# Performance work log

Measured on AMD Instinct MI355X. Metric: run time of the kernel, lower is better.

## Reference

```python
import jax, jax.numpy as jnp
import numpy as np

D_MODEL = 1024
N_HEADS = 16
D_HEAD = D_MODEL // N_HEADS
B, S = 4, 2048


def setup_inputs() -> dict:
    key = jax.random.key(0)
    ks = jax.random.split(key, 12)
    std = 1.0 / np.sqrt(D_MODEL)
    inp = {
        "q": jax.random.normal(ks[0], (B, S, D_MODEL), jnp.float32),
        "k": jax.random.normal(ks[1], (B, S, D_MODEL), jnp.float32),
        "v": jax.random.normal(ks[2], (B, S, D_MODEL), jnp.float32),
        # causal mask: 1 where attention is disallowed (j > i)
        "mask": jnp.triu(jnp.ones((S, S), jnp.int32), k=1)[None, None],
        "Wq": jax.random.normal(ks[3], (D_MODEL, D_MODEL), jnp.float32) * std,
        "bq": jnp.zeros((D_MODEL,), jnp.float32),
        "Wk": jax.random.normal(ks[4], (D_MODEL, D_MODEL), jnp.float32) * std,
        "bk": jnp.zeros((D_MODEL,), jnp.float32),
        "Wv": jax.random.normal(ks[5], (D_MODEL, D_MODEL), jnp.float32) * std,
        "bv": jnp.zeros((D_MODEL,), jnp.float32),
        "Wo": jax.random.normal(ks[6], (D_MODEL, D_MODEL), jnp.float32) * std,
        "bo": jnp.zeros((D_MODEL,), jnp.float32),
    }
    return inp


def _split_heads(x):
    # [B, S, D] -> [B, H, S, d_head]
    b, s, _ = x.shape
    return x.reshape(b, s, N_HEADS, D_HEAD).transpose(0, 2, 1, 3)


def reference(q, k, v, mask, Wq, bq, Wk, bk, Wv, bv, Wo, bo):
    # torch Linear: y = x @ W.T + b
    qh = _split_heads(q @ Wq.T + bq)
    kh = _split_heads(k @ Wk.T + bk)
    vh = _split_heads(v @ Wv.T + bv)
    # NOTE: original scales by sqrt(d_model), not sqrt(d_head)
    scale = 1.0 / np.sqrt(D_MODEL).astype(np.float32)
    logits = jnp.einsum("bhqd,bhkd->bhqk", qh, kh) * scale
    logits = logits + mask.astype(logits.dtype) * (-1e9)
    weights = jax.nn.softmax(logits, axis=-1)
    attn = jnp.einsum("bhqk,bhkd->bhqd", weights, vh)
    attn = attn.transpose(0, 2, 1, 3).reshape(q.shape[0], -1, D_MODEL)
    out = attn @ Wo.T + bo
    return out, weights
```

## Files before the change

### kernel.cpp

```cpp
#include <hip/hip_runtime.h>
#include <stdint.h>

typedef unsigned short u16;
typedef __attribute__((ext_vector_type(8))) short bf16x8;
typedef __attribute__((ext_vector_type(8))) unsigned short us8;
typedef __attribute__((ext_vector_type(4))) float f32x4;

typedef __attribute__((address_space(1))) void as1_void;
typedef __attribute__((address_space(3))) void as3_void;

#define S_LEN 2048
#define DMODEL 1024
#define DH 64
#define NHEADS 16
#define NB 4
#define GM (NB * S_LEN)
#define GN DMODEL
#define GK DMODEL
#define SCALE 0.03125f

__device__ __forceinline__ void gload16(const void* g, void* l) {
  __builtin_amdgcn_global_load_lds((const as1_void*)g, (as3_void*)l, 16, 0, 0);
}
__device__ __forceinline__ float bf2f(u16 u) {
  union { unsigned int i; float f; } x; x.i = ((unsigned int)u) << 16; return x.f;
}
__device__ __forceinline__ u16 f2bf(float f) {
  union { float f; unsigned int i; } x; x.f = f;
  unsigned int u = x.i + 0x7fffu + ((x.i >> 16) & 1u);
  return (u16)(u >> 16);
}
__device__ __forceinline__ f32x4 mfma16(bf16x8 a, bf16x8 b, f32x4 c) {
  return __builtin_amdgcn_mfma_f32_16x16x32_bf16(a, b, c, 0, 0, 0);
}
__device__ __forceinline__ void nt_store4(f32x4 v, float* p) {
  __builtin_nontemporal_store(v, (f32x4*)p);
}

__device__ __forceinline__ void cvt_chunk(const float* s, u16* d, int i) {
  const f32x4 a = *(const f32x4*)(s + (size_t)i * 8);
  const f32x4 b = *(const f32x4*)(s + (size_t)i * 8 + 4);
  us8 o;
  o[0] = f2bf(a[0]); o[1] = f2bf(a[1]); o[2] = f2bf(a[2]); o[3] = f2bf(a[3]);
  o[4] = f2bf(b[0]); o[5] = f2bf(b[1]); o[6] = f2bf(b[2]); o[7] = f2bf(b[3]);
  *(us8*)(d + (size_t)i * 8) = o;
}
__global__ __launch_bounds__(256)
void cvt3(const float* __restrict__ s0, const float* __restrict__ s1,
          const float* __restrict__ s2, u16* __restrict__ d0,
          u16* __restrict__ d1, u16* __restrict__ d2, int n8) {
  const int i = blockIdx.x * 256 + threadIdx.x;
  if (i >= n8) return;
  const float* s; u16* d;
  if (blockIdx.y == 0)      { s = s0; d = d0; }
  else if (blockIdx.y == 1) { s = s1; d = d1; }
  else                      { s = s2; d = d2; }
  cvt_chunk(s, d, i);
}
__global__ __launch_bounds__(256)
void cvt4(const float* __restrict__ s0, const float* __restrict__ s1,
          const float* __restrict__ s2, const float* __restrict__ s3,
          u16* __restrict__ d0, u16* __restrict__ d1,
          u16* __restrict__ d2, u16* __restrict__ d3, int n8) {
  const int i = blockIdx.x * 256 + threadIdx.x;
  if (i >= n8) return;
  const float* s; u16* d;
  if (blockIdx.y == 0)      { s = s0; d = d0; }
  else if (blockIdx.y == 1) { s = s1; d = d1; }
  else if (blockIdx.y == 2) { s = s2; d = d2; }
  else                      { s = s3; d = d3; }
  cvt_chunk(s, d, i);
}

template<bool OUTF>
__device__ __forceinline__ void gemm_body(const u16* __restrict__ A,
                                          const u16* __restrict__ W,
                                          const float* __restrict__ bias,
                                          void* __restrict__ Cv,
                                          u16* smem) {
  u16* As = smem;
  u16* Bs = smem + 2 * 8192;
  const int tid  = threadIdx.x;
  const int lane = tid & 63;
  const int wv   = tid >> 6;
  const int wr   = wv >> 1, wc = wv & 1;
  const int rlow = lane & 15, rhi = lane >> 4;
  const int m0 = blockIdx.x * 128;
  const int n0 = blockIdx.y * 128;

  f32x4 acc[4][4];
#pragma unroll
  for (int i = 0; i < 4; ++i)
#pragma unroll
    for (int j = 0; j < 4; ++j) acc[i][j] = (f32x4){0.f, 0.f, 0.f, 0.f};

#define STAGE_G(bufi, kk)                                                     \
  {                                                                           \
    _Pragma("unroll")                                                         \
    for (int i = 0; i < 4; ++i) {                                             \
      const int c = i * 256 + tid;                                            \
      const int row = c >> 3, cw = c & 7;                                     \
      const int koff = ((kk) << 6) + ((cw ^ (row & 7)) << 3);                 \
      gload16(A + (size_t)(m0 + row) * GK + koff,                             \
              &As[(bufi) * 8192 + ((c - lane) << 3)]);                        \
      gload16(W + (size_t)(n0 + row) * GK + koff,                             \
              &Bs[(bufi) * 8192 + ((c - lane) << 3)]);                        \
    }                                                                         \
  }

  const int nk = GK >> 6;
  STAGE_G(0, 0);
  __syncthreads();
  int buf = 0;
  for (int kk = 0; kk < nk; ++kk) {
    if (kk + 1 < nk) STAGE_G(buf ^ 1, kk + 1);
    const u16* Ab = &As[buf * 8192];
    const u16* Bb = &Bs[buf * 8192];
    bf16x8 af[4][2], bfr[4][2];
#pragma unroll
    for (int mi = 0; mi < 4; ++mi) {
      const int row = wr * 64 + mi * 16 + rlow;
#pragma unroll
      for (int k2 = 0; k2 < 2; ++k2)
        af[mi][k2] = *(const bf16x8*)&Ab[row * 64 + (((rhi + k2 * 4) ^ (row & 7)) << 3)];
    }
#pragma unroll
    for (int ni = 0; ni < 4; ++ni) {
      const int row = wc * 64 + ni * 16 + rlow;
#pragma unroll
      for (int k2 = 0; k2 < 2; ++k2)
        bfr[ni][k2] = *(const bf16x8*)&Bb[row * 64 + (((rhi + k2 * 4) ^ (row & 7)) << 3)];
    }
#pragma unroll
    for (int mi = 0; mi < 4; ++mi)
#pragma unroll
      for (int ni = 0; ni < 4; ++ni) {
        acc[mi][ni] = mfma16(af[mi][0], bfr[ni][0], acc[mi][ni]);
        acc[mi][ni] = mfma16(af[mi][1], bfr[ni][1], acc[mi][ni]);
      }
    __syncthreads();
    buf ^= 1;
  }
#undef STAGE_G

  if constexpr (OUTF) {
    float* Cs = (float*)smem;
#pragma unroll
    for (int ni = 0; ni < 4; ++ni) {
      const int col = wc * 64 + ni * 16 + rlow;
      const float bv = bias[n0 + col];
#pragma unroll
      for (int mi = 0; mi < 4; ++mi)
#pragma unroll
        for (int r = 0; r < 4; ++r)
          Cs[(wr * 64 + mi * 16 + rhi * 4 + r) * 128 + col] = acc[mi][ni][r] + bv;
    }
    __syncthreads();
#pragma unroll
    for (int i = 0; i < 16; ++i) {
      const int c = i * 256 + tid;
      const int row = c >> 5, cw = c & 31;
      const f32x4 t = *(const f32x4*)&Cs[row * 128 + cw * 4];
      nt_store4(t, &((float*)Cv)[(size_t)(m0 + row) * GN + n0 + cw * 4]);
    }
  } else {
    u16* Cs = smem;
#pragma unroll
    for (int ni = 0; ni < 4; ++ni) {
      const int col = wc * 64 + ni * 16 + rlow;
      const float bv = bias[n0 + col];
#pragma unroll
      for (int mi = 0; mi < 4; ++mi)
#pragma unroll
        for (int r = 0; r < 4; ++r)
          Cs[(wr * 64 + mi * 16 + rhi * 4 + r) * 144 + col] = f2bf(acc[mi][ni][r] + bv);
    }
    __syncthreads();
#pragma unroll
    for (int i = 0; i < 8; ++i) {
      const int c = i * 256 + tid;
      const int row = c >> 4, cw = c & 15;
      const us8 t = *(const us8*)&Cs[row * 144 + cw * 8];
      *(us8*)&((u16*)Cv)[(size_t)(m0 + row) * GN + n0 + cw * 8] = t;
    }
  }
}

__global__ __launch_bounds__(256, 2)
void gemm_qkv(const u16* __restrict__ xq, const u16* __restrict__ xk,
              const u16* __restrict__ xv, const u16* __restrict__ wq,
              const u16* __restrict__ wk, const u16* __restrict__ wv,
              const float* __restrict__ bq, const float* __restrict__ bk,
              const float* __restrict__ bv, u16* __restrict__ oq,
              u16* __restrict__ ok, u16* __restrict__ ov) {
  __shared__ u16 smem[4 * 8192];
  const u16 *A, *W; const float* bias; u16* C;
  if (blockIdx.z == 0)      { A = xq; W = wq; bias = bq; C = oq; }
  else if (blockIdx.z == 1) { A = xk; W = wk; bias = bk; C = ok; }
  else                      { A = xv; W = wv; bias = bv; C = ov; }
  gemm_body<false>(A, W, bias, C, smem);
}

__global__ __launch_bounds__(256, 2)
void gemm_o(const u16* __restrict__ A, const u16* __restrict__ W,
            const float* __restrict__ bias, float* __restrict__ C) {
  __shared__ u16 smem[4 * 8192];
  gemm_body<true>(A, W, bias, C, smem);
}

__global__ __launch_bounds__(512, 4)
void attn_fused(const u16* __restrict__ qh, const u16* __restrict__ kh,
                const u16* __restrict__ vh, float* __restrict__ wout,
                u16* __restrict__ am)
{
  __shared__ u16 smem[34304];
  u16* Ws  = smem;
  u16* Qs  = smem;
  u16* Kb1 = smem;
  u16* Kb0 = smem + 17408;
  u16* VT  = smem + 17408 + 8192;

  const int tid = threadIdx.x, lane = tid & 63, wv = tid >> 6;
  const int rlow = lane & 15, rhi = lane >> 4;
  const int idx = blockIdx.x;
  const int bh  = idx & 63;
  const int qt  = 15 - (idx >> 6);
  const int b = bh >> 4, h = bh & 15;
  const int q0 = qt << 7;
  const size_t headoff = (size_t)b * S_LEN * DMODEL + h * DH;

#define STAGE_K(dst, jtile)                                                   \
  {                                                                           \
    _Pragma("unroll")                                                         \
    for (int i = 0; i < 2; ++i) {                                             \
      const int c = i * 512 + tid;                                            \
      const int row = c >> 3, cw = c & 7;                                     \
      gload16(kh + headoff + (size_t)((jtile) * 128 + row) * DMODEL +         \
              ((cw ^ (row & 7)) << 3), &(dst)[(c - lane) << 3]);              \
    }                                                                         \
  }

#pragma unroll
  for (int i = 0; i < 2; ++i) {
    const int c = i * 512 + tid;
    const int row = c >> 3, cw = c & 7;
    gload16(qh + headoff + (size_t)(q0 + row) * DMODEL + ((cw ^ (row & 7)) << 3),
            &Qs[(c - lane) << 3]);
  }
  __syncthreads();
  bf16x8 qf[2];
  {
    const int row = wv * 16 + rlow;
#pragma unroll
    for (int k2 = 0; k2 < 2; ++k2)
      qf[k2] = *(const bf16x8*)&Qs[row * 64 + (((rhi + k2 * 4) ^ (row & 7)) << 3)];
  }

  const int gi_base = q0 + wv * 16 + rhi * 4;
  float ssum[4] = {0.f, 0.f, 0.f, 0.f};

  STAGE_K(Kb0, 0);
  for (int jt = 0; jt <= qt; ++jt) {
    __syncthreads();
    const u16* kcur = (jt & 1) ? Kb1 : Kb0;
    if (jt < qt) {
      u16* knxt = (jt & 1) ? Kb0 : Kb1;
      STAGE_K(knxt, jt + 1);
    }
    const bool diag = (jt == qt);
    float pexp[4] = {0.f, 0.f, 0.f, 0.f};
#pragma unroll
    for (int half = 0; half < 2; ++half) {
      f32x4 acc[4];
#pragma unroll
      for (int ni = 0; ni < 4; ++ni) acc[ni] = (f32x4){0.f, 0.f, 0.f, 0.f};
#pragma unroll
      for (int k2 = 0; k2 < 2; ++k2) {
#pragma unroll
        for (int ni = 0; ni < 4; ++ni) {
          const int row = (half * 4 + ni) * 16 + rlow;
          bf16x8 kf = *(const bf16x8*)&kcur[row * 64 + (((rhi + k2 * 4) ^ (row & 7)) << 3)];
          acc[ni] = mfma16(qf[k2], kf, acc[ni]);
        }
      }
#pragma unroll
      for (int ni = 0; ni < 4; ++ni) {
        const int gj = jt * 128 + (half * 4 + ni) * 16 + rlow;
#pragma unroll
        for (int r = 0; r < 4; ++r) {
          if (!diag || gj <= gi_base + r) pexp[r] += __expf(acc[ni][r] * SCALE);
        }
      }
    }
#pragma unroll
    for (int r = 0; r < 4; ++r) {
      float p = pexp[r];
      p += __shfl_xor(p, 1);
      p += __shfl_xor(p, 2);
      p += __shfl_xor(p, 4);
      p += __shfl_xor(p, 8);
      ssum[r] += p;
    }
  }
  float inv_s[4];
#pragma unroll
  for (int r = 0; r < 4; ++r) inv_s[r] = 1.f / ssum[r];

  f32x4 opv[4];
#pragma unroll
  for (int ni = 0; ni < 4; ++ni) opv[ni] = (f32x4){0.f, 0.f, 0.f, 0.f};

  for (int jt = 0; jt <= qt; ++jt) {
    __syncthreads();
    STAGE_K(Kb0, jt);
#pragma unroll
    for (int i = 0; i < 2; ++i) {
      const int j = (i << 6) | lane;
      const int d0v = wv << 3;
      bf16x8 vv = *(const bf16x8*)(vh + headoff + (size_t)(jt * 128 + j) * DMODEL + d0v);
#pragma unroll
      for (int e = 0; e < 8; ++e) VT[(d0v + e) * 136 + j] = (u16)vv[e];
    }
    __syncthreads();
    const bool diag = (jt == qt);
#pragma unroll
    for (int half = 0; half < 2; ++half) {
      f32x4 acc[4];
#pragma unroll
      for (int ni = 0; ni < 4; ++ni) acc[ni] = (f32x4){0.f, 0.f, 0.f, 0.f};
#pragma unroll
      for (int k2 = 0; k2 < 2; ++k2) {
#pragma unroll
        for (int ni = 0; ni < 4; ++ni) {
          const int row = (half * 4 + ni) * 16 + rlow;
          bf16x8 kf = *(const bf16x8*)&Kb0[row * 64 + (((rhi + k2 * 4) ^ (row & 7)) << 3)];
          acc[ni] = mfma16(qf[k2], kf, acc[ni]);
        }
      }
#pragma unroll
      for (int ni = 0; ni < 4; ++ni) {
        const int col = (half * 4 + ni) * 16 + rlow;
        const int gj = jt * 128 + col;
#pragma unroll
        for (int r = 0; r < 4; ++r) {
          float w = 0.f;
          if (!diag || gj <= gi_base + r) w = __expf(acc[ni][r] * SCALE) * inv_s[r];
          Ws[(wv * 16 + rhi * 4 + r) * 136 + col] = f2bf(w);
        }
      }
    }
    __syncthreads();
    {
      const size_t wbase = ((size_t)bh * S_LEN + q0) * S_LEN + (size_t)jt * 128;
#pragma unroll
      for (int i = 0; i < 8; ++i) {
        const int c = i * 512 + tid;
        const int row = c >> 5, cw = c & 31;
        f32x4 t;
        t[0] = bf2f(Ws[row * 136 + cw * 4 + 0]);
        t[1] = bf2f(Ws[row * 136 + cw * 4 + 1]);
        t[2] = bf2f(Ws[row * 136 + cw * 4 + 2]);
        t[3] = bf2f(Ws[row * 136 + cw * 4 + 3]);
        nt_store4(t, wout + wbase + (size_t)row * S_LEN + cw * 4);
      }
    }
#pragma unroll
    for (int k4 = 0; k4 < 4; ++k4) {
      const bf16x8 afr = *(const bf16x8*)&Ws[(wv * 16 + rlow) * 136 + rhi * 8 + k4 * 32];
#pragma unroll
      for (int ni = 0; ni < 4; ++ni) {
        const bf16x8 vfr = *(const bf16x8*)&VT[(ni * 16 + rlow) * 136 + rhi * 8 + k4 * 32];
        opv[ni] = mfma16(afr, vfr, opv[ni]);
      }
    }
  }
#undef STAGE_K

  {
    const f32x4 z = {0.f, 0.f, 0.f, 0.f};
    for (int jt = qt + 1; jt < 16; ++jt) {
      const size_t wbase = ((size_t)bh * S_LEN + q0) * S_LEN + (size_t)jt * 128;
#pragma unroll
      for (int i = 0; i < 8; ++i) {
        const int c = i * 512 + tid;
        const int row = c >> 5, cw = c & 31;
        nt_store4(z, wout + wbase + (size_t)row * S_LEN + cw * 4);
      }
    }
  }

  __syncthreads();
  {
    u16* Os = smem;
#pragma unroll
    for (int ni = 0; ni < 4; ++ni)
#pragma unroll
      for (int r = 0; r < 4; ++r)
        Os[(wv * 16 + rhi * 4 + r) * 72 + ni * 16 + rlow] = f2bf(opv[ni][r]);
    __syncthreads();
#pragma unroll
    for (int i = 0; i < 2; ++i) {
      const int c = i * 512 + tid;
      const int row = c >> 3, cw = c & 7;
      const us8 t = *(const us8*)&Os[row * 72 + cw * 8];
      *(us8*)(am + headoff + (size_t)(q0 + row) * DMODEL + cw * 8) = t;
    }
  }
}

extern "C" void kernel_launch(void* const* d_in, const int* in_sizes, int n_in,
                              void* d_out, int out_size, void* d_ws, size_t ws_size,
                              hipStream_t stream) {
  const float* q  = (const float*)d_in[0];
  const float* k  = (const float*)d_in[1];
  const float* v  = (const float*)d_in[2];
  const float* Wq = (const float*)d_in[4];
  const float* bq = (const float*)d_in[5];
  const float* Wk = (const float*)d_in[6];
  const float* bk = (const float*)d_in[7];
  const float* Wv = (const float*)d_in[8];
  const float* bv = (const float*)d_in[9];
  const float* Wo = (const float*)d_in[10];
  const float* bo = (const float*)d_in[11];

  const size_t proj_elems = (size_t)NB * S_LEN * DMODEL;
  const size_t w_elems    = (size_t)DMODEL * DMODEL;
  float* out0 = (float*)d_out;
  float* wts  = out0 + proj_elems;

  u16* qh  = (u16*)d_ws;
  u16* kh  = qh + proj_elems;
  u16* vh  = kh + proj_elems;
  u16* am  = vh + proj_elems;
  u16* wco = am + proj_elems;

  u16* xq = (u16*)wts;
  u16* xk = xq + proj_elems;
  u16* xv = xk + proj_elems;
  u16* wq_ = xv + proj_elems;
  u16* wk_ = wq_ + w_elems;
  u16* wv_ = wk_ + w_elems;

  const int n8x = (int)(proj_elems / 8);
  const int n8w = (int)(w_elems / 8);

  cvt3<<<dim3(n8x / 256, 3), dim3(256), 0, stream>>>(q, k, v, xq, xk, xv, n8x);
  cvt4<<<dim3(n8w / 256, 4), dim3(256), 0, stream>>>(Wq, Wk, Wv, Wo,
                                                     wq_, wk_, wv_, wco, n8w);
  gemm_qkv<<<dim3(64, 8, 3), dim3(256), 0, stream>>>(xq, xk, xv, wq_, wk_, wv_,
                                                     bq, bk, bv, qh, kh, vh);
  attn_fused<<<dim3(1024), dim3(512), 0, stream>>>(qh, kh, vh, wts, am);
  gemm_o<<<dim3(64, 8), dim3(256), 0, stream>>>(am, wco, bo, out0);
}
```

Before: 355.7 us.

## Move causal-mask zero-fill of attention weights into projection GEMM kernels

The zero-filling of upper-triangular attention-weight tiles is removed from the attention kernel and spread across extra blocks interleaved in the QKV and output projection GEMM launches. The bandwidth-bound store work runs alongside compute-bound GEMM blocks instead of serialising at the end of attention blocks. The converted weights are relocated into the output buffer so the bf16 staging areas do not overlap tiles being zeroed during the QKV GEMM. The change adds index arithmetic with a small while loop per tile, and depends on correct buffer aliasing: zeroing must not overwrite staging data still in use.

```diff
diff --git a/kernel.cpp b/kernel.cpp
--- a/kernel.cpp
+++ b/kernel.cpp
@@ -72,12 +72,29 @@
   cvt_chunk(s, d, i);
 }
 
+__device__ __forceinline__ void zero_tiles(float* __restrict__ wz, int tid,
+                                           int zi, int bh_base, int tmax,
+                                           int stride) {
+  const f32x4 z4 = {0.f, 0.f, 0.f, 0.f};
+  for (int t = zi; t < tmax; t += stride) {
+    const int bh = bh_base + t / 120;
+    int r = t % 120;
+    int i = 0;
+    while (r >= 15 - i) { r -= 15 - i; ++i; }
+    const int j = i + 1 + r;
+    float* p = wz + ((size_t)(bh * 2048 + i * 128)) * 2048 + j * 128;
+#pragma unroll 4
+    for (int c = tid; c < 4096; c += 256)
+      nt_store4(z4, p + (size_t)(c >> 5) * 2048 + ((c & 31) << 2));
+  }
+}
+
 template<bool OUTF>
 __device__ __forceinline__ void gemm_body(const u16* __restrict__ A,
                                           const u16* __restrict__ W,
                                           const float* __restrict__ bias,
                                           void* __restrict__ Cv,
-                                          u16* smem) {
+                                          u16* smem, int m0, int n0) {
   u16* As = smem;
   u16* Bs = smem + 2 * 8192;
   const int tid  = threadIdx.x;
@@ -85,8 +102,6 @@
   const int wv   = tid >> 6;
   const int wr   = wv >> 1, wc = wv & 1;
   const int rlow = lane & 15, rhi = lane >> 4;
-  const int m0 = blockIdx.x * 128;
-  const int n0 = blockIdx.y * 128;
 
   f32x4 acc[4][4];
 #pragma unroll
@@ -187,25 +202,42 @@
 }
 
 __global__ __launch_bounds__(256, 2)
-void gemm_qkv(const u16* __restrict__ xq, const u16* __restrict__ xk,
-              const u16* __restrict__ xv, const u16* __restrict__ wq,
-              const u16* __restrict__ wk, const u16* __restrict__ wv,
-              const float* __restrict__ bq, const float* __restrict__ bk,
-              const float* __restrict__ bv, u16* __restrict__ oq,
-              u16* __restrict__ ok, u16* __restrict__ ov) {
+void gemm_qkv_z(const u16* __restrict__ xq, const u16* __restrict__ xk,
+                const u16* __restrict__ xv, const u16* __restrict__ wq,
+                const u16* __restrict__ wk, const u16* __restrict__ wv,
+                const float* __restrict__ bq, const float* __restrict__ bk,
+                const float* __restrict__ bv, u16* __restrict__ oq,
+                u16* __restrict__ ok, u16* __restrict__ ov,
+                float* __restrict__ wz) {
   __shared__ u16 smem[4 * 8192];
+  const int bid = blockIdx.x;
+  if ((bid & 3) == 3) {
+    zero_tiles(wz, threadIdx.x, bid >> 2, 3, 7320, 512);
+    return;
+  }
+  const int gi = (bid >> 2) * 3 + (bid & 3);
+  const int z = gi >> 9, rr = gi & 511;
+  const int m0 = (rr & 63) * 128, n0 = (rr >> 6) * 128;
   const u16 *A, *W; const float* bias; u16* C;
-  if (blockIdx.z == 0)      { A = xq; W = wq; bias = bq; C = oq; }
-  else if (blockIdx.z == 1) { A = xk; W = wk; bias = bk; C = ok; }
-  else                      { A = xv; W = wv; bias = bv; C = ov; }
-  gemm_body<false>(A, W, bias, C, smem);
+  if (z == 0)      { A = xq; W = wq; bias = bq; C = oq; }
+  else if (z == 1) { A = xk; W = wk; bias = bk; C = ok; }
+  else             { A = xv; W = wv; bias = bv; C = ov; }
+  gemm_body<false>(A, W, bias, C, smem, m0, n0);
 }
 
 __global__ __launch_bounds__(256, 2)
-void gemm_o(const u16* __restrict__ A, const u16* __restrict__ W,
-            const float* __restrict__ bias, float* __restrict__ C) {
+void gemm_o_z(const u16* __restrict__ A, const u16* __restrict__ W,
+              const float* __restrict__ bias, float* __restrict__ C,
+              float* __restrict__ wz) {
   __shared__ u16 smem[4 * 8192];
-  gemm_body<true>(A, W, bias, C, smem);
+  const int bid = blockIdx.x;
+  if (bid % 5 == 4) {
+    zero_tiles(wz, threadIdx.x, bid / 5, 0, 360, 128);
+    return;
+  }
+  const int gi = (bid / 5) * 4 + (bid % 5);
+  const int m0 = (gi & 63) * 128, n0 = (gi >> 6) * 128;
+  gemm_body<true>(A, W, bias, C, smem, m0, n0);
 }
 
 __global__ __launch_bounds__(512, 4)
@@ -375,19 +407,6 @@
     }
   }
 #undef STAGE_K
-
-  {
-    const f32x4 z = {0.f, 0.f, 0.f, 0.f};
-    for (int jt = qt + 1; jt < 16; ++jt) {
-      const size_t wbase = ((size_t)bh * S_LEN + q0) * S_LEN + (size_t)jt * 128;
-#pragma unroll
-      for (int i = 0; i < 8; ++i) {
-        const int c = i * 512 + tid;
-        const int row = c >> 5, cw = c & 31;
-        nt_store4(z, wout + wbase + (size_t)row * S_LEN + cw * 4);
-      }
-    }
-  }
 
   __syncthreads();
   {
@@ -437,7 +456,7 @@
   u16* xq = (u16*)wts;
   u16* xk = xq + proj_elems;
   u16* xv = xk + proj_elems;
-  u16* wq_ = xv + proj_elems;
+  u16* wq_ = (u16*)out0;
   u16* wk_ = wq_ + w_elems;
   u16* wv_ = wk_ + w_elems;
 
@@ -447,8 +466,8 @@
   cvt3<<<dim3(n8x / 256, 3), dim3(256), 0, stream>>>(q, k, v, xq, xk, xv, n8x);
   cvt4<<<dim3(n8w / 256, 4), dim3(256), 0, stream>>>(Wq, Wk, Wv, Wo,
                                                      wq_, wk_, wv_, wco, n8w);
-  gemm_qkv<<<dim3(64, 8, 3), dim3(256), 0, stream>>>(xq, xk, xv, wq_, wk_, wv_,
-                                                     bq, bk, bv, qh, kh, vh);
+  gemm_qkv_z<<<dim3(2048), dim3(256), 0, stream>>>(xq, xk, xv, wq_, wk_, wv_,
+                                                   bq, bk, bv, qh, kh, vh, wts);
   attn_fused<<<dim3(1024), dim3(512), 0, stream>>>(qh, kh, vh, wts, am);
-  gemm_o<<<dim3(64, 8), dim3(256), 0, stream>>>(am, wco, bo, out0);
-}
+  gemm_o_z<<<dim3(640), dim3(256), 0, stream>>>(am, wco, bo, out0, wts);
+}
```

Result: slower. 419.0 us (+17.8%).
